# Kernel tuning notes

Measured on AMD Instinct MI355X. Metric: run time of the kernel, lower is better.

Reference implementation:

```python
import jax, jax.numpy as jnp
import numpy as np

H = 64          # hiddens_dims
K = 3           # Chebyshev order
B = 16          # graphs in batch
NPG = 16384     # nodes per graph
N = B * NPG     # total nodes
E = 2_097_152   # total edges
R = 2191        # num_residues (hard-coded in source)
E_REF = R * 16
HALF = N // 2   # backbone count == sidechain count (mask is balanced per graph)


def _lin(k, fan_in, shape):
    return jax.random.uniform(k, shape, jnp.float32, -1.0, 1.0) / np.sqrt(fan_in)


def setup_inputs() -> dict:
    key = jax.random.key(0)
    ks = jax.random.split(key, 40)
    inp = {}
    inp["x"] = jax.random.normal(ks[0], (N, 3), jnp.float32)
    inp["edge_index"] = jax.random.randint(ks[1], (2, E), 0, N)
    inp["batch"] = jnp.repeat(jnp.arange(B, dtype=jnp.int32), NPG)
    blk = jnp.concatenate([jnp.ones((NPG // 2,), bool), jnp.zeros((NPG // 2,), bool)])
    inp["mask"] = jnp.tile(blk, B)  # backbone=True first half of each graph block
    inp["x_ref"] = jax.random.normal(ks[2], (R, 3), jnp.float32)
    inp["edgeref"] = jax.random.randint(ks[3], (2, E_REF), 0, R)
    i = 4
    for name, cin in [("cw0", 3), ("cw1", H), ("cw2", H), ("rw0", 3), ("rw1", H), ("rw2", H)]:
        inp[name] = _lin(ks[i], cin, (K, cin, H)); i += 1
        inp[name.replace("w", "b")] = jnp.zeros((H,), jnp.float32)  # ChebConv bias init = zeros
    for name, cin, cout in [("mlp_w", 2 * H, H), ("mlpP2_w", 2 * H, H),
                            ("rep0_w", H, H), ("rep1_w", H, H), ("rep2_w", H, 3)]:
        inp[name] = _lin(ks[i], cin, (cin, cout)); i += 1
        inp[name.replace("_w", "_b")] = _lin(ks[i], cin, (cout,)); i += 1
    return inp


def cheb_conv(x, edge_index, W, b, n):
    # PyG ChebConv with sym normalization, lambda_max=2: L_hat = -D^-1/2 A D^-1/2 (diag = 0)
    row, col = edge_index[0], edge_index[1]
    deg = jax.ops.segment_sum(jnp.ones_like(x[:, 0])[row] * 0 + 1.0, row, num_segments=n)
    dinv = jnp.where(deg > 0, jax.lax.rsqrt(jnp.maximum(deg, 1e-12)), 0.0)
    w = -(dinv[row] * dinv[col])  # [E]

    def prop(h):  # L_hat @ h via gather + segment_sum
        return jax.ops.segment_sum(w[:, None] * h[col], row, num_segments=n)

    Tx0 = x
    out = Tx0 @ W[0]
    Tx1 = prop(x)
    out = out + Tx1 @ W[1]
    for k in range(2, K):
        Tx2 = 2.0 * prop(Tx1) - Tx0
        out = out + Tx2 @ W[k]
        Tx0, Tx1 = Tx1, Tx2
    return out + b


def _forward(x, edge_index, mask, x_ref, edgeref,
             cw0, cb0, cw1, cb1, cw2, cb2, rw0, rb0, rw1, rb1, rw2, rb2,
             mlp_w, mlp_b, mlpP2_w, mlpP2_b,
             rep0_w, rep0_b, rep1_w, rep1_b, rep2_w, rep2_b):
    # main GNN stack (tanh after all but last; dropout is identity in eval)
    h = jnp.tanh(cheb_conv(x, edge_index, cw0, cb0, N))
    h = jnp.tanh(cheb_conv(h, edge_index, cw1, cb1, N))
    h = cheb_conv(h, edge_index, cw2, cb2, N)

    bb_idx = jnp.nonzero(mask, size=HALF)[0]
    sc_idx = jnp.nonzero(~mask, size=HALF)[0]
    x_bb = h[bb_idx].reshape(B, -1, H).mean(axis=1)[:, None, :]  # [B,1,H]
    x_sc = h[sc_idx].reshape(B, -1, H).mean(axis=1)[:, None, :]  # [B,1,H]

    # reference-graph stack: source bug makes `conv2 != self.convs[-1]` always True,
    # so tanh follows every convRef layer
    r = jnp.tanh(cheb_conv(x_ref, edgeref, rw0, rb0, R))
    r = jnp.tanh(cheb_conv(r, edgeref, rw1, rb1, R))
    r = jnp.tanh(cheb_conv(r, edgeref, rw2, rb2, R))
    r = jnp.broadcast_to(r[None], (B, R, H))

    bb_rep = jnp.broadcast_to(x_bb, (B, R, H))
    phase1 = jnp.concatenate([r, bb_rep], axis=-1) @ mlp_w + mlp_b        # [B,R,H]
    sc_rep = jnp.broadcast_to(x_sc, (B, R, H))
    phase2 = jnp.concatenate([phase1, sc_rep], axis=-1) @ mlpP2_w + mlpP2_b  # [B,R,H]

    res = phase2.reshape(-1, H)
    res = jax.nn.relu(res @ rep0_w + rep0_b)
    res = jax.nn.relu(res @ rep1_w + rep1_b)
    res = jax.nn.relu(res @ rep2_w + rep2_b)  # [B*R, 3]
    return res.reshape(-1, 3), x_bb, x_sc


def reference(x, edge_index, batch, mask, x_ref, edgeref,
              cw0, cb0, cw1, cb1, cw2, cb2, rw0, rb0, rw1, rb1, rw2, rb2,
              mlp_w, mlp_b, mlpP2_w, mlpP2_b,
              rep0_w, rep0_b, rep1_w, rep1_b, rep2_w, rep2_b):
    del batch  # only used for len(batch.unique()) == B, a static constant here
    return _forward(x, edge_index, mask, x_ref, edgeref,
                    cw0, cb0, cw1, cb1, cw2, cb2, rw0, rb0, rw1, rb1, rw2, rb2,
                    mlp_w, mlp_b, mlpP2_w, mlpP2_b,
                    rep0_w, rep0_b, rep1_w, rep1_b, rep2_w, rep2_b)
```

## Files before the change

### kernel.cpp

```cpp
#include <hip/hip_runtime.h>
#include <hip/hip_fp16.h>
#include <math.h>

#define NN 262144
#define NE 2097152
#define RR 2191
#define ER (RR*16)
#define NB 16
#define BRR (NB*RR)
#define OUT_RES (BRR*3)

typedef __attribute__((ext_vector_type(8))) _Float16 half8;
typedef __attribute__((ext_vector_type(4))) float f32x4;

__global__ void k_hist2(const int* __restrict__ eM, int* __restrict__ degM,
                        unsigned char* __restrict__ rankM,
                        const int* __restrict__ eR, int* __restrict__ degR,
                        unsigned char* __restrict__ rankR){
  int b = blockIdx.x;
  if (b < 2048){
    for (int i = b*256 + threadIdx.x; i < NE; i += 2048*256){
      int old = atomicAdd(&degM[eM[i]], 1);
      rankM[i] = (unsigned char)old;
    }
  } else {
    for (int i = (b-2048)*256 + threadIdx.x; i < ER; i += 64*256){
      int old = atomicAdd(&degR[eR[i]], 1);
      rankR[i] = (unsigned char)old;
    }
  }
}

__global__ void k_scan1(const int* __restrict__ deg, int* __restrict__ rowptr,
                        int* __restrict__ partials, float* __restrict__ dinv){
  __shared__ int s[256];
  int t = threadIdx.x; int i = blockIdx.x*256 + t;
  int v = deg[i]; s[t] = v; __syncthreads();
  dinv[i] = v > 0 ? 1.0f/sqrtf((float)v) : 0.0f;
  for (int off = 1; off < 256; off <<= 1){
    int x = (t >= off) ? s[t-off] : 0; __syncthreads();
    s[t] += x; __syncthreads();
  }
  rowptr[i] = s[t] - v;
  if (t == 255) partials[blockIdx.x] = s[255];
}

__global__ void __launch_bounds__(1024) k_scan2m(int* __restrict__ partials,
                                                 const int* __restrict__ degR,
                                                 int* __restrict__ rowptrR,
                                                 float* __restrict__ dinvR){
  __shared__ int s[1024];
  int t = threadIdx.x;
  if (blockIdx.x == 0){
    int v = partials[t]; s[t] = v; __syncthreads();
    for (int off = 1; off < 1024; off <<= 1){
      int x = (t >= off) ? s[t-off] : 0; __syncthreads();
      s[t] += x; __syncthreads();
    }
    partials[t] = s[t] - v;
  } else {
    int carry = 0;
    for (int base = 0; base < RR; base += 1024){
      int idx = base + t;
      int v = (idx < RR) ? degR[idx] : 0;
      if (idx < RR) dinvR[idx] = v > 0 ? 1.0f/sqrtf((float)v) : 0.0f;
      s[t] = v; __syncthreads();
      for (int off = 1; off < 1024; off <<= 1){
        int x = (t >= off) ? s[t-off] : 0; __syncthreads();
        s[t] += x; __syncthreads();
      }
      if (idx < RR) rowptrR[idx] = carry + s[t] - v;
      carry += s[1023];
      __syncthreads();
    }
    if (t == 0) rowptrR[RR] = carry;
  }
}

__global__ void k_scan3(int* __restrict__ rowptr, const int* __restrict__ partials){
  int t = threadIdx.x; int i = blockIdx.x*256 + t;
  rowptr[i] += partials[blockIdx.x];
  if (i == 0) rowptr[NN] = NE;
}

__global__ void k_scatter2(const int* __restrict__ eM, const float* __restrict__ dinv,
                           const int* __restrict__ rowptr, const unsigned char* __restrict__ rankM,
                           int2* __restrict__ pair,
                           const int* __restrict__ eR, const float* __restrict__ dinvR,
                           const int* __restrict__ rowptrR, const unsigned char* __restrict__ rankR,
                           int2* __restrict__ pairR){
  int b = blockIdx.x;
  if (b < 2048){
    for (int i = b*256 + threadIdx.x; i < NE; i += 2048*256){
      int r = eM[i], c = eM[NE + i];
      int pos = rowptr[r] + rankM[i];
      unsigned wbits = (unsigned)__float_as_int(-dinv[r]*dinv[c]);
      long long v = (unsigned)c | ((long long)wbits << 32);
      __builtin_nontemporal_store(v, (long long*)(pair + pos));
    }
  } else {
    for (int i = (b-2048)*256 + threadIdx.x; i < ER; i += 64*256){
      int r = eR[i], c = eR[ER + i];
      int pos = rowptrR[r] + rankR[i];
      unsigned wbits = (unsigned)__float_as_int(-dinvR[r]*dinvR[c]);
      long long v = (unsigned)c | ((long long)wbits << 32);
      __builtin_nontemporal_store(v, (long long*)(pairR + pos));
    }
  }
}

__global__ void k_prep(const float* __restrict__ cw1, const float* __restrict__ cw2,
                       const float* __restrict__ rw1, const float* __restrict__ rw2,
                       float* __restrict__ weffC2, float* __restrict__ weffR1,
                       float* __restrict__ weffR2, _Float16* __restrict__ wfragC1,
                       const float* __restrict__ x, float4* __restrict__ x4,
                       const float* __restrict__ x_ref, float4* __restrict__ xr4){
  int y = blockIdx.y;
  int i = blockIdx.x*blockDim.x + threadIdx.x;
  if (y < 3){
    if (i < 4096){
      const float* W = (y == 0) ? cw2 : (y == 1) ? rw1 : rw2;
      float* D       = (y == 0) ? weffC2 : (y == 1) ? weffR1 : weffR2;
      D[i]        = W[i] - W[8192 + i];
      D[4096 + i] = W[4096 + i];
      D[8192 + i] = 2.0f * W[8192 + i];
    }
  } else if (y == 3){
    if (i < 12288){
      int reg = i & 7, lane = (i >> 3) & 63, nt = (i >> 9) & 3, kc = i >> 11;
      int m = kc >> 1;
      int kin = (kc & 1)*32 + ((lane >> 4) & 3)*8 + reg;
      int n = nt*16 + (lane & 15);
      float eff;
      if      (m == 0) eff = cw1[kin*64 + n] - cw1[8192 + kin*64 + n];
      else if (m == 1) eff = cw1[4096 + kin*64 + n];
      else             eff = 2.0f * cw1[8192 + kin*64 + n];
      wfragC1[i] = (_Float16)eff;
    }
  } else if (y == 4){
    if (i < NN) x4[i] = make_float4(x[i*3], x[i*3+1], x[i*3+2], 0.0f);
  } else {
    if (i < RR) xr4[i] = make_float4(x_ref[i*3], x_ref[i*3+1], x_ref[i*3+2], 0.0f);
  }
}

__global__ void k_prop3p(const float4* __restrict__ h, float4* __restrict__ y,
                         const int* __restrict__ rowptr, const int2* __restrict__ pair, int n){
  int i = blockIdx.x*blockDim.x + threadIdx.x;
  if (i >= n) return;
  float a0 = 0.f, a1 = 0.f, a2 = 0.f;
  int s = rowptr[i], e = rowptr[i+1];
  int p = s;
  for (; p + 4 <= e; p += 4){
    int2 q0 = pair[p], q1 = pair[p+1], q2 = pair[p+2], q3 = pair[p+3];
    float4 v0 = h[q0.x], v1 = h[q1.x], v2 = h[q2.x], v3 = h[q3.x];
    float w0 = __int_as_float(q0.y), w1 = __int_as_float(q1.y);
    float w2 = __int_as_float(q2.y), w3 = __int_as_float(q3.y);
    a0 = fmaf(w0,v0.x, fmaf(w1,v1.x, fmaf(w2,v2.x, fmaf(w3,v3.x, a0))));
    a1 = fmaf(w0,v0.y, fmaf(w1,v1.y, fmaf(w2,v2.y, fmaf(w3,v3.y, a1))));
    a2 = fmaf(w0,v0.z, fmaf(w1,v1.z, fmaf(w2,v2.z, fmaf(w3,v3.z, a2))));
  }
  for (; p < e; p++){
    int2 q = pair[p]; float wv = __int_as_float(q.y);
    float4 v = h[q.x];
    a0 = fmaf(wv, v.x, a0); a1 = fmaf(wv, v.y, a1); a2 = fmaf(wv, v.z, a2);
  }
  y[i] = make_float4(a0, a1, a2, 0.0f);
}

__global__ void k_prop64(const float* __restrict__ h, float* __restrict__ y,
                         const int* __restrict__ rowptr, const int2* __restrict__ pair, int n){
  int t = threadIdx.x, lane = t & 63;
  int i = blockIdx.x*4 + (t >> 6);
  if (i >= n) return;
  float acc = 0.f;
  int s = rowptr[i], e = rowptr[i+1];
  int p = s;
  for (; p + 4 <= e; p += 4){
    int2 q0 = pair[p], q1 = pair[p+1], q2 = pair[p+2], q3 = pair[p+3];
    float v0 = h[(size_t)q0.x*64 + lane], v1 = h[(size_t)q1.x*64 + lane];
    float v2 = h[(size_t)q2.x*64 + lane], v3 = h[(size_t)q3.x*64 + lane];
    acc = fmaf(__int_as_float(q0.y),v0, fmaf(__int_as_float(q1.y),v1,
          fmaf(__int_as_float(q2.y),v2, fmaf(__int_as_float(q3.y),v3, acc))));
  }
  for (; p < e; p++){
    int2 q = pair[p];
    acc = fmaf(__int_as_float(q.y), h[(size_t)q.x*64 + lane], acc);
  }
  y[(size_t)i*64 + lane] = acc;
}

__global__ void __launch_bounds__(256) k_prop64h(
    const uint4* __restrict__ h4, uint4* __restrict__ y4,
    const int* __restrict__ rowptr, const int2* __restrict__ pair, int n){
  int t = threadIdx.x;
  int sub = t & 7;
  int row = blockIdx.x*32 + (t >> 3);
  if (row >= n) return;
  int s = rowptr[row], e = rowptr[row+1];
  float ac[8];
  #pragma unroll
  for (int k = 0; k < 8; k++) ac[k] = 0.f;
  int p = s;
  for (; p + 8 <= e; p += 8){
    int2 q[8]; uint4 v[8];
    #pragma unroll
    for (int j = 0; j < 8; j++) q[j] = pair[p+j];
    #pragma unroll
    for (int j = 0; j < 8; j++) v[j] = h4[(size_t)q[j].x*8 + sub];
    #pragma unroll
    for (int j = 0; j < 8; j++){
      float wv = __int_as_float(q[j].y);
      #pragma unroll
      for (int k = 0; k < 4; k++){
        float2 f = __half22float2(((const __half2*)&v[j])[k]);
        ac[2*k]   = fmaf(wv, f.x, ac[2*k]);
        ac[2*k+1] = fmaf(wv, f.y, ac[2*k+1]);
      }
    }
  }
  for (; p + 4 <= e; p += 4){
    int2 q[4]; uint4 v[4];
    #pragma unroll
    for (int j = 0; j < 4; j++) q[j] = pair[p+j];
    #pragma unroll
    for (int j = 0; j < 4; j++) v[j] = h4[(size_t)q[j].x*8 + sub];
    #pragma unroll
    for (int j = 0; j < 4; j++){
      float wv = __int_as_float(q[j].y);
      #pragma unroll
      for (int k = 0; k < 4; k++){
        float2 f = __half22float2(((const __half2*)&v[j])[k]);
        ac[2*k]   = fmaf(wv, f.x, ac[2*k]);
        ac[2*k+1] = fmaf(wv, f.y, ac[2*k+1]);
      }
    }
  }
  for (; p < e; p++){
    int2 q = pair[p];
    float wv = __int_as_float(q.y);
    uint4 v = h4[(size_t)q.x*8 + sub];
    #pragma unroll
    for (int k = 0; k < 4; k++){
      float2 f = __half22float2(((const __half2*)&v)[k]);
      ac[2*k]   = fmaf(wv, f.x, ac[2*k]);
      ac[2*k+1] = fmaf(wv, f.y, ac[2*k+1]);
    }
  }
  uint4 r;
  #pragma unroll
  for (int k = 0; k < 4; k++){
    __half2 hp = __floats2half2_rn(ac[2*k], ac[2*k+1]);
    ((unsigned*)&r)[k] = *(unsigned*)&hp;
  }
  y4[(size_t)row*8 + sub] = r;
}

__global__ void k_combine3f(const float4* __restrict__ x, const float4* __restrict__ t1,
                            const float4* __restrict__ t2, const float* __restrict__ W,
                            const float* __restrict__ bias, float* __restrict__ out, int n){
  int t = threadIdx.x, lane = t & 63;
  int i = blockIdx.x*4 + (t >> 6);
  if (i >= n) return;
  float4 px = x[i], p1 = t1[i], p2 = t2[i];
  const float* fx = (const float*)&px;
  const float* f1 = (const float*)&p1;
  const float* f2 = (const float*)&p2;
  float acc = bias[lane];
  #pragma unroll
  for (int j = 0; j < 3; j++){
    float x0 = fx[j], x1 = f1[j];
    float x2 = 2.0f*f2[j] - x0;
    acc += x0*W[      j*64 + lane]
         + x1*W[192 + j*64 + lane]
         + x2*W[384 + j*64 + lane];
  }
  out[(size_t)i*64 + lane] = tanhf(acc);
}

__global__ void k_combine3h(const float4* __restrict__ x, const float4* __restrict__ t1,
                            const float4* __restrict__ t2, const float* __restrict__ W,
                            const float* __restrict__ bias, __half* __restrict__ out, int n){
  int t = threadIdx.x, lane = t & 63;
  int i = blockIdx.x*4 + (t >> 6);
  if (i >= n) return;
  float4 px = x[i], p1 = t1[i], p2 = t2[i];
  const float* fx = (const float*)&px;
  const float* f1 = (const float*)&p1;
  const float* f2 = (const float*)&p2;
  float acc = bias[lane];
  #pragma unroll
  for (int j = 0; j < 3; j++){
    float x0 = fx[j], x1 = f1[j];
    float x2 = 2.0f*f2[j] - x0;
    acc += x0*W[      j*64 + lane]
         + x1*W[192 + j*64 + lane]
         + x2*W[384 + j*64 + lane];
  }
  out[(size_t)i*64 + lane] = __float2half_rn(tanhf(acc));
}

__global__ void __launch_bounds__(256) k_combine64m(
    const __half* A, const __half* B, const __half* C,
    const _Float16* __restrict__ wfrag, const float* __restrict__ bias,
    __half* out, int ntiles, int wavestride){
  int t = threadIdx.x;
  int lane = t & 63;
  int wv = blockIdx.x*4 + (t >> 6);
  half8 bf[24];
  #pragma unroll
  for (int i = 0; i < 24; i++)
    bf[i] = *(const half8*)(wfrag + ((size_t)(i*64 + lane))*8);
  int col = lane & 15, grp = (lane >> 4) & 3;
  float b0 = bias[col], b1 = bias[16+col], b2 = bias[32+col], b3 = bias[48+col];
  for (int tile = wv; tile < ntiles; tile += wavestride){
    size_t rb = (size_t)tile*16;
    f32x4 acc0 = {b0,b0,b0,b0}, acc1 = {b1,b1,b1,b1};
    f32x4 acc2 = {b2,b2,b2,b2}, acc3 = {b3,b3,b3,b3};
    #pragma unroll
    for (int kc = 0; kc < 6; kc++){
      const __half* s = (kc < 2) ? A : (kc < 4) ? B : C;
      half8 a = *(const half8*)(s + (rb + col)*64 + (kc & 1)*32 + grp*8);
      acc0 = __builtin_amdgcn_mfma_f32_16x16x32_f16(a, bf[kc*4+0], acc0, 0,0,0);
      acc1 = __builtin_amdgcn_mfma_f32_16x16x32_f16(a, bf[kc*4+1], acc1, 0,0,0);
      acc2 = __builtin_amdgcn_mfma_f32_16x16x32_f16(a, bf[kc*4+2], acc2, 0,0,0);
      acc3 = __builtin_amdgcn_mfma_f32_16x16x32_f16(a, bf[kc*4+3], acc3, 0,0,0);
    }
    __half* o = out + (rb + grp*4)*64;
    #pragma unroll
    for (int r = 0; r < 4; r++){
      o[(size_t)r*64 +      col] = __float2half_rn(tanhf(acc0[r]));
      o[(size_t)r*64 + 16 + col] = __float2half_rn(tanhf(acc1[r]));
      o[(size_t)r*64 + 32 + col] = __float2half_rn(tanhf(acc2[r]));
      o[(size_t)r*64 + 48 + col] = __float2half_rn(tanhf(acc3[r]));
    }
  }
}

__global__ void k_pool3(const __half2* __restrict__ hA, const __half2* __restrict__ hB,
                        const __half2* __restrict__ hC, float* __restrict__ pA,
                        float* __restrict__ pB, float* __restrict__ pC){
  const __half2* src = (blockIdx.y == 0) ? hA : (blockIdx.y == 1) ? hB : hC;
  float* dst         = (blockIdx.y == 0) ? pA : (blockIdx.y == 1) ? pB : pC;
  int blk = blockIdx.x;
  int chunk = blk & 15, seg = blk >> 4;
  int t = threadIdx.x, ch2 = t & 31, rsub = t >> 5;
  int base = seg*8192 + chunk*512;
  float ax = 0.f, ay = 0.f;
  for (int j = 0; j < 64; j++){
    int row = base + rsub + j*8;
    float2 v = __half22float2(src[(size_t)row*32 + ch2]);
    ax += v.x; ay += v.y;
  }
  __shared__ float sx[256], sy[256];
  sx[t] = ax; sy[t] = ay; __syncthreads();
  if (t < 32){
    float tx = 0.f, ty = 0.f;
    #pragma unroll
    for (int j = 0; j < 8; j++){ tx += sx[ch2 + j*32]; ty += sy[ch2 + j*32]; }
    int b = seg >> 1, half_ = seg & 1;
    atomicAdd(&dst[half_*1024 + b*64 + ch2*2],     tx);
    atomicAdd(&dst[half_*1024 + b*64 + ch2*2 + 1], ty);
  }
}

__global__ void k_combine_pooled(const float* __restrict__ pA, const float* __restrict__ pB,
                                 const float* __restrict__ pC, const float* __restrict__ weff,
                                 const float* __restrict__ bias, float* __restrict__ xbbsc,
                                 float* __restrict__ dout){
  int i = blockIdx.x*blockDim.x + threadIdx.x;
  int pr = i >> 6, c = i & 63;
  const float* a = pA + pr*64;
  const float* b = pB + pr*64;
  const float* cc = pC + pr*64;
  float v = 0.f;
  for (int k = 0; k < 64; k++){
    v = fmaf(a[k],  weff[        k*64 + c], v);
    v = fmaf(b[k],  weff[4096 +  k*64 + c], v);
    v = fmaf(cc[k], weff[8192 +  k*64 + c], v);
  }
  v = v*(1.0f/8192.0f) + bias[c];
  xbbsc[i] = v;
  dout[OUT_RES + i] = v;
}

__global__ void __launch_bounds__(256) k_combine64f(
    const float* __restrict__ A, const float* __restrict__ Bm, const float* __restrict__ C,
    const float* __restrict__ Weff, const float* __restrict__ bias,
    float* __restrict__ out, int n){
  int t = threadIdx.x;
  int lane = t & 63;
  int wid  = __builtin_amdgcn_readfirstlane(t >> 6);
  int half_ = wid & 1;
  int row  = blockIdx.x*128 + (wid >> 1)*64 + lane;
  bool active = (row < n);
  float acc[32];
  #pragma unroll
  for (int c = 0; c < 32; c++) acc[c] = bias[half_*32 + c];
  if (active){
    #pragma unroll 1
    for (int m = 0; m < 3; m++){
      const float* src = (m == 0 ? A : (m == 1 ? Bm : C)) + (size_t)row*64;
      const float* Wm  = Weff + m*4096 + half_*32;
      #pragma unroll 1
      for (int k4 = 0; k4 < 16; k4++){
        float4 a4 = *(const float4*)(src + k4*4);
        const float* wk = Wm + k4*256;
        #pragma unroll
        for (int kk = 0; kk < 4; kk++){
          float a = (kk == 0) ? a4.x : (kk == 1) ? a4.y : (kk == 2) ? a4.z : a4.w;
          #pragma unroll
          for (int c = 0; c < 32; c++)
            acc[c] = fmaf(a, wk[kk*64 + c], acc[c]);
        }
      }
    }
  }
  __syncthreads();
  if (active){
    float* o = out + (size_t)row*64 + half_*32;
    #pragma unroll
    for (int c = 0; c < 32; c++) o[c] = tanhf(acc[c]);
  }
}

__global__ void k_refchain(const float* __restrict__ refA, const float* __restrict__ mlp_w,
                           const float* __restrict__ mlp2_w, const float* __restrict__ rep0_w,
                           float* __restrict__ rt3a, int n){
  int t = threadIdx.x, lane = t & 63;
  int i = blockIdx.x*4 + (t >> 6);
  if (i >= n) return;
  float v = refA[i*64 + lane];
  float a = 0.f;
  #pragma unroll
  for (int k = 0; k < 64; k++) a += __shfl(v, k, 64) * mlp_w[k*64 + lane];
  float b = 0.f;
  #pragma unroll
  for (int k = 0; k < 64; k++) b += __shfl(a, k, 64) * mlp2_w[k*64 + lane];
  float c = 0.f;
  #pragma unroll
  for (int k = 0; k < 64; k++) c += __shfl(b, k, 64) * rep0_w[k*64 + lane];
  rt3a[i*64 + lane] = c;
}

__global__ void k_bbchain(const float* __restrict__ xbbsc,
                          const float* __restrict__ mlp_w,  const float* __restrict__ mlp_b,
                          const float* __restrict__ mlp2_w, const float* __restrict__ mlp2_b,
                          const float* __restrict__ rep0_w, const float* __restrict__ rep0_b,
                          float* __restrict__ bt3a){
  int t = threadIdx.x, lane = t & 63;
  int i = blockIdx.x*4 + (t >> 6);
  if (i >= NB) return;
  float vbb = xbbsc[i*64 + lane];
  float vsc = xbbsc[1024 + i*64 + lane];
  float a = mlp_b[lane];
  #pragma unroll
  for (int k = 0; k < 64; k++) a += __shfl(vbb, k, 64) * mlp_w[4096 + k*64 + lane];
  float b = mlp2_b[lane];
  #pragma unroll
  for (int k = 0; k < 64; k++) b += __shfl(a, k, 64) * mlp2_w[k*64 + lane];
  #pragma unroll
  for (int k = 0; k < 64; k++) b += __shfl(vsc, k, 64) * mlp2_w[4096 + k*64 + lane];
  float c = rep0_b[lane];
  #pragma unroll
  for (int k = 0; k < 64; k++) c += __shfl(b, k, 64) * rep0_w[k*64 + lane];
  bt3a[i*64 + lane] = c;
}

__global__ void k_final(const float* __restrict__ rt3, const float* __restrict__ bt3,
                        const float* __restrict__ W1, const float* __restrict__ b1,
                        const float* __restrict__ W2, const float* __restrict__ b2,
                        float* __restrict__ dout){
  int t = threadIdx.x, lane = t & 63;
  int g = blockIdx.x*4 + (t >> 6);
  if (g >= BRR) return;
  int b = g / RR, r = g - b*RR;
  float m = rt3[r*64 + lane] + bt3[b*64 + lane];
  m = fmaxf(m, 0.0f);
  float acc = b1[lane];
  #pragma unroll
  for (int k = 0; k < 64; k++) acc += __shfl(m, k, 64) * W1[k*64 + lane];
  float u = fmaxf(acc, 0.0f);
  float p0 = u*W2[lane*3+0], p1 = u*W2[lane*3+1], p2 = u*W2[lane*3+2];
  #pragma unroll
  for (int off = 32; off > 0; off >>= 1){
    p0 += __shfl_xor(p0, off, 64);
    p1 += __shfl_xor(p1, off, 64);
    p2 += __shfl_xor(p2, off, 64);
  }
  if (lane == 0){
    dout[g*3+0] = fmaxf(p0 + b2[0], 0.0f);
    dout[g*3+1] = fmaxf(p1 + b2[1], 0.0f);
    dout[g*3+2] = fmaxf(p2 + b2[2], 0.0f);
  }
}

extern "C" void kernel_launch(void* const* d_in, const int* in_sizes, int n_in,
                              void* d_out, int out_size, void* d_ws, size_t ws_size,
                              hipStream_t stream){
  const float* x     = (const float*)d_in[0];
  const int*   eidx  = (const int*)d_in[1];
  const float* x_ref = (const float*)d_in[4];
  const int*   eref  = (const int*)d_in[5];
  const float* cw0 = (const float*)d_in[6],  *cb0 = (const float*)d_in[7];
  const float* cw1 = (const float*)d_in[8],  *cb1 = (const float*)d_in[9];
  const float* cw2 = (const float*)d_in[10], *cb2 = (const float*)d_in[11];
  const float* rw0 = (const float*)d_in[12], *rb0 = (const float*)d_in[13];
  const float* rw1 = (const float*)d_in[14], *rb1 = (const float*)d_in[15];
  const float* rw2 = (const float*)d_in[16], *rb2 = (const float*)d_in[17];
  const float* mlp_w  = (const float*)d_in[18], *mlp_b  = (const float*)d_in[19];
  const float* mlp2_w = (const float*)d_in[20], *mlp2_b = (const float*)d_in[21];
  const float* rep0_w = (const float*)d_in[22], *rep0_b = (const float*)d_in[23];
  const float* rep1_w = (const float*)d_in[24], *rep1_b = (const float*)d_in[25];
  const float* rep2_w = (const float*)d_in[26], *rep2_b = (const float*)d_in[27];
  float* out = (float*)d_out;

  char* w = (char*)d_ws;
  size_t off = 0;
  auto alloc = [&](size_t bytes)->void*{
    void* p = w + off;
    off = (off + bytes + 255) & ~(size_t)255;
    return p;
  };
  int*   deg     = (int*)  alloc(NN*4);
  int*   degR    = (int*)  alloc(RR*4);
  float* poolA   = (float*)alloc(2048*4);
  float* poolB   = (float*)alloc(2048*4);
  float* poolC   = (float*)alloc(2048*4);
  size_t zero_bytes = off;

  int*   rowptr   = (int*)  alloc((NN+1)*4);
  int*   partials = (int*)  alloc(1024*4);
  int*   rowptrR  = (int*)  alloc((RR+1)*4);
  float* dinv     = (float*)alloc(NN*4);
  float* dinvR    = (float*)alloc(RR*4);
  unsigned char* rankM = (unsigned char*)alloc(NE);
  unsigned char* rankR = (unsigned char*)alloc(ER);
  int2*  cpair    = (int2*) alloc((size_t)NE*8);
  int2*  cpairR   = (int2*) alloc((size_t)ER*8);
  float4* x4      = (float4*)alloc((size_t)NN*16);
  float4* t1_4    = (float4*)alloc((size_t)NN*16);
  float4* t2_4    = (float4*)alloc((size_t)NN*16);
  float4* xr4     = (float4*)alloc((size_t)RR*16);
  float4* rt1_4   = (float4*)alloc((size_t)RR*16);
  float4* rt2_4   = (float4*)alloc((size_t)RR*16);
  __half* hA      = (__half*)alloc((size_t)NN*64*2);
  __half* hB      = (__half*)alloc((size_t)NN*64*2);
  __half* hC      = (__half*)alloc((size_t)NN*64*2);
  float* refA     = (float*)alloc(RR*64*4);
  float* refB     = (float*)alloc(RR*64*4);
  float* refC     = (float*)alloc(RR*64*4);
  float* xbbsc    = (float*)alloc(2048*4);
  float* rt3a     = (float*)alloc(RR*64*4);
  float* bt3a     = (float*)alloc(NB*64*4);
  float* weffC2   = (float*)alloc(12288*4);
  float* weffR1   = (float*)alloc(12288*4);
  float* weffR2   = (float*)alloc(12288*4);
  _Float16* wfragC1 = (_Float16*)alloc(12288*2);
  (void)ws_size; (void)in_sizes; (void)n_in; (void)out_size;

  hipMemsetAsync(d_ws, 0, zero_bytes, stream);

  k_prep<<<dim3(1024, 6), 256, 0, stream>>>(cw1, cw2, rw1, rw2,
                                            weffC2, weffR1, weffR2, wfragC1,
                                            x, x4, x_ref, xr4);

  k_hist2<<<2112, 256, 0, stream>>>(eidx, deg, rankM, eref, degR, rankR);
  k_scan1<<<1024, 256, 0, stream>>>(deg, rowptr, partials, dinv);
  k_scan2m<<<2, 1024, 0, stream>>>(partials, degR, rowptrR, dinvR);
  k_scan3<<<1024, 256, 0, stream>>>(rowptr, partials);
  k_scatter2<<<2112, 256, 0, stream>>>(eidx, dinv, rowptr, rankM, cpair,
                                       eref, dinvR, rowptrR, rankR, cpairR);

  k_prop3p<<<1024, 256, 0, stream>>>(x4, t1_4, rowptr, cpair, NN);
  k_prop3p<<<1024, 256, 0, stream>>>(t1_4, t2_4, rowptr, cpair, NN);
  k_combine3h<<<NN/4, 256, 0, stream>>>(x4, t1_4, t2_4, cw0, cb0, hA, NN);
  k_prop64h<<<NN/32, 256, 0, stream>>>((const uint4*)hA, (uint4*)hB, rowptr, cpair, NN);
  k_prop64h<<<NN/32, 256, 0, stream>>>((const uint4*)hB, (uint4*)hC, rowptr, cpair, NN);
  k_combine64m<<<1024, 256, 0, stream>>>(hA, hB, hC, wfragC1, cb1, hA, NN/16, 4096);
  k_prop64h<<<NN/32, 256, 0, stream>>>((const uint4*)hA, (uint4*)hB, rowptr, cpair, NN);
  k_prop64h<<<NN/32, 256, 0, stream>>>((const uint4*)hB, (uint4*)hC, rowptr, cpair, NN);
  k_pool3<<<dim3(512,3), 256, 0, stream>>>((const __half2*)hA, (const __half2*)hB,
                                           (const __half2*)hC, poolA, poolB, poolC);
  k_combine_pooled<<<8, 256, 0, stream>>>(poolA, poolB, poolC, weffC2, cb2, xbbsc, out);

  k_prop3p<<<9, 256, 0, stream>>>(xr4, rt1_4, rowptrR, cpairR, RR);
  k_prop3p<<<9, 256, 0, stream>>>(rt1_4, rt2_4, rowptrR, cpairR, RR);
  k_combine3f<<<548, 256, 0, stream>>>(xr4, rt1_4, rt2_4, rw0, rb0, refA, RR);
  k_prop64<<<548, 256, 0, stream>>>(refA, refB, rowptrR, cpairR, RR);
  k_prop64<<<548, 256, 0, stream>>>(refB, refC, rowptrR, cpairR, RR);
  k_combine64f<<<(RR+127)/128, 256, 0, stream>>>(refA, refB, refC, weffR1, rb1, refA, RR);
  k_prop64<<<548, 256, 0, stream>>>(refA, refB, rowptrR, cpairR, RR);
  k_prop64<<<548, 256, 0, stream>>>(refB, refC, rowptrR, cpairR, RR);
  k_combine64f<<<(RR+127)/128, 256, 0, stream>>>(refA, refB, refC, weffR2, rb2, refA, RR);

  k_refchain<<<548, 256, 0, stream>>>(refA, mlp_w, mlp2_w, rep0_w, rt3a, RR);
  k_bbchain<<<4, 256, 0, stream>>>(xbbsc, mlp_w, mlp_b, mlp2_w, mlp2_b, rep0_w, rep0_b, bt3a);

  k_final<<<(BRR+3)/4, 256, 0, stream>>>(rt3a, bt3a, rep1_w, rep1_b, rep2_w, rep2_b, out);
}
```

Before: 724.1 us.

## Merge main-graph and reference-graph kernels into shared launches

Kernels for the large batched graph and the small reference graph that run at the same stage are merged into single launches, with blocks dispatched by block index. The prep work is folded into the histogram kernel in the same way. This cuts the kernel count roughly in half, removing launch overhead and the serialized small reference-graph kernels that left most of the GPU idle. The cost is branchier kernels and possible register-pressure or occupancy changes from combining different bodies.

```diff
diff --git a/kernel.cpp b/kernel.cpp
--- a/kernel.cpp
+++ b/kernel.cpp
@@ -13,21 +13,52 @@
 typedef __attribute__((ext_vector_type(8))) _Float16 half8;
 typedef __attribute__((ext_vector_type(4))) float f32x4;
 
-__global__ void k_hist2(const int* __restrict__ eM, int* __restrict__ degM,
-                        unsigned char* __restrict__ rankM,
-                        const int* __restrict__ eR, int* __restrict__ degR,
-                        unsigned char* __restrict__ rankR){
-  int b = blockIdx.x;
+__global__ void k_histprep(const int* __restrict__ eM, int* __restrict__ degM,
+                           unsigned char* __restrict__ rankM,
+                           const int* __restrict__ eR, int* __restrict__ degR,
+                           unsigned char* __restrict__ rankR,
+                           const float* __restrict__ cw1, const float* __restrict__ cw2,
+                           const float* __restrict__ rw1, const float* __restrict__ rw2,
+                           float* __restrict__ weffC2, float* __restrict__ weffR1,
+                           float* __restrict__ weffR2, _Float16* __restrict__ wfragC1,
+                           const float* __restrict__ x, float4* __restrict__ x4,
+                           const float* __restrict__ x_ref, float4* __restrict__ xr4){
+  int b = blockIdx.x, t = threadIdx.x;
   if (b < 2048){
-    for (int i = b*256 + threadIdx.x; i < NE; i += 2048*256){
+    for (int i = b*256 + t; i < NE; i += 2048*256){
       int old = atomicAdd(&degM[eM[i]], 1);
       rankM[i] = (unsigned char)old;
     }
-  } else {
-    for (int i = (b-2048)*256 + threadIdx.x; i < ER; i += 64*256){
+  } else if (b < 2112){
+    for (int i = (b-2048)*256 + t; i < ER; i += 64*256){
       int old = atomicAdd(&degR[eR[i]], 1);
       rankR[i] = (unsigned char)old;
     }
+  } else if (b < 2160){
+    int y = (b - 2112) >> 4;
+    int i = ((b - 2112) & 15)*256 + t;
+    const float* W = (y == 0) ? cw2 : (y == 1) ? rw1 : rw2;
+    float* D       = (y == 0) ? weffC2 : (y == 1) ? weffR1 : weffR2;
+    D[i]        = W[i] - W[8192 + i];
+    D[4096 + i] = W[4096 + i];
+    D[8192 + i] = 2.0f * W[8192 + i];
+  } else if (b < 2208){
+    int i = (b - 2160)*256 + t;
+    int reg = i & 7, lane = (i >> 3) & 63, nt = (i >> 9) & 3, kc = i >> 11;
+    int m = kc >> 1;
+    int kin = (kc & 1)*32 + ((lane >> 4) & 3)*8 + reg;
+    int n = nt*16 + (lane & 15);
+    float eff;
+    if      (m == 0) eff = cw1[kin*64 + n] - cw1[8192 + kin*64 + n];
+    else if (m == 1) eff = cw1[4096 + kin*64 + n];
+    else             eff = 2.0f * cw1[8192 + kin*64 + n];
+    wfragC1[i] = (_Float16)eff;
+  } else if (b < 3232){
+    int i = (b - 2208)*256 + t;
+    if (i < NN) x4[i] = make_float4(x[i*3], x[i*3+1], x[i*3+2], 0.0f);
+  } else {
+    int i = (b - 3232)*256 + t;
+    if (i < RR) xr4[i] = make_float4(x_ref[i*3], x_ref[i*3+1], x_ref[i*3+2], 0.0f);
   }
 }
 
@@ -109,45 +140,9 @@
   }
 }
 
-__global__ void k_prep(const float* __restrict__ cw1, const float* __restrict__ cw2,
-                       const float* __restrict__ rw1, const float* __restrict__ rw2,
-                       float* __restrict__ weffC2, float* __restrict__ weffR1,
-                       float* __restrict__ weffR2, _Float16* __restrict__ wfragC1,
-                       const float* __restrict__ x, float4* __restrict__ x4,
-                       const float* __restrict__ x_ref, float4* __restrict__ xr4){
-  int y = blockIdx.y;
-  int i = blockIdx.x*blockDim.x + threadIdx.x;
-  if (y < 3){
-    if (i < 4096){
-      const float* W = (y == 0) ? cw2 : (y == 1) ? rw1 : rw2;
-      float* D       = (y == 0) ? weffC2 : (y == 1) ? weffR1 : weffR2;
-      D[i]        = W[i] - W[8192 + i];
-      D[4096 + i] = W[4096 + i];
-      D[8192 + i] = 2.0f * W[8192 + i];
-    }
-  } else if (y == 3){
-    if (i < 12288){
-      int reg = i & 7, lane = (i >> 3) & 63, nt = (i >> 9) & 3, kc = i >> 11;
-      int m = kc >> 1;
-      int kin = (kc & 1)*32 + ((lane >> 4) & 3)*8 + reg;
-      int n = nt*16 + (lane & 15);
-      float eff;
-      if      (m == 0) eff = cw1[kin*64 + n] - cw1[8192 + kin*64 + n];
-      else if (m == 1) eff = cw1[4096 + kin*64 + n];
-      else             eff = 2.0f * cw1[8192 + kin*64 + n];
-      wfragC1[i] = (_Float16)eff;
-    }
-  } else if (y == 4){
-    if (i < NN) x4[i] = make_float4(x[i*3], x[i*3+1], x[i*3+2], 0.0f);
-  } else {
-    if (i < RR) xr4[i] = make_float4(x_ref[i*3], x_ref[i*3+1], x_ref[i*3+2], 0.0f);
-  }
-}
-
-__global__ void k_prop3p(const float4* __restrict__ h, float4* __restrict__ y,
-                         const int* __restrict__ rowptr, const int2* __restrict__ pair, int n){
-  int i = blockIdx.x*blockDim.x + threadIdx.x;
-  if (i >= n) return;
+__device__ __forceinline__ void prop3_body(const float4* __restrict__ h, float4* __restrict__ y,
+                                           const int* __restrict__ rowptr,
+                                           const int2* __restrict__ pair, int i){
   float a0 = 0.f, a1 = 0.f, a2 = 0.f;
   int s = rowptr[i], e = rowptr[i+1];
   int p = s;
@@ -168,11 +163,31 @@
   y[i] = make_float4(a0, a1, a2, 0.0f);
 }
 
-__global__ void k_prop64(const float* __restrict__ h, float* __restrict__ y,
-                         const int* __restrict__ rowptr, const int2* __restrict__ pair, int n){
-  int t = threadIdx.x, lane = t & 63;
-  int i = blockIdx.x*4 + (t >> 6);
-  if (i >= n) return;
+__device__ __forceinline__ void combine3_body(const float4* __restrict__ x,
+                                              const float4* __restrict__ t1,
+                                              const float4* __restrict__ t2,
+                                              const float* __restrict__ W,
+                                              const float* __restrict__ bias,
+                                              int i, int lane, float* accout){
+  float4 px = x[i], p1 = t1[i], p2 = t2[i];
+  const float* fx = (const float*)&px;
+  const float* f1 = (const float*)&p1;
+  const float* f2 = (const float*)&p2;
+  float acc = bias[lane];
+  #pragma unroll
+  for (int j = 0; j < 3; j++){
+    float x0 = fx[j], x1 = f1[j];
+    float x2 = 2.0f*f2[j] - x0;
+    acc += x0*W[      j*64 + lane]
+         + x1*W[192 + j*64 + lane]
+         + x2*W[384 + j*64 + lane];
+  }
+  *accout = tanhf(acc);
+}
+
+__device__ __forceinline__ void prop64f_body(const float* __restrict__ h, float* __restrict__ y,
+                                             const int* __restrict__ rowptr,
+                                             const int2* __restrict__ pair, int i, int lane){
   float acc = 0.f;
   int s = rowptr[i], e = rowptr[i+1];
   int p = s;
@@ -190,209 +205,17 @@
   y[(size_t)i*64 + lane] = acc;
 }
 
-__global__ void __launch_bounds__(256) k_prop64h(
-    const uint4* __restrict__ h4, uint4* __restrict__ y4,
-    const int* __restrict__ rowptr, const int2* __restrict__ pair, int n){
-  int t = threadIdx.x;
-  int sub = t & 7;
-  int row = blockIdx.x*32 + (t >> 3);
-  if (row >= n) return;
-  int s = rowptr[row], e = rowptr[row+1];
-  float ac[8];
-  #pragma unroll
-  for (int k = 0; k < 8; k++) ac[k] = 0.f;
-  int p = s;
-  for (; p + 8 <= e; p += 8){
-    int2 q[8]; uint4 v[8];
-    #pragma unroll
-    for (int j = 0; j < 8; j++) q[j] = pair[p+j];
-    #pragma unroll
-    for (int j = 0; j < 8; j++) v[j] = h4[(size_t)q[j].x*8 + sub];
-    #pragma unroll
-    for (int j = 0; j < 8; j++){
-      float wv = __int_as_float(q[j].y);
-      #pragma unroll
-      for (int k = 0; k < 4; k++){
-        float2 f = __half22float2(((const __half2*)&v[j])[k]);
-        ac[2*k]   = fmaf(wv, f.x, ac[2*k]);
-        ac[2*k+1] = fmaf(wv, f.y, ac[2*k+1]);
-      }
-    }
-  }
-  for (; p + 4 <= e; p += 4){
-    int2 q[4]; uint4 v[4];
-    #pragma unroll
-    for (int j = 0; j < 4; j++) q[j] = pair[p+j];
-    #pragma unroll
-    for (int j = 0; j < 4; j++) v[j] = h4[(size_t)q[j].x*8 + sub];
-    #pragma unroll
-    for (int j = 0; j < 4; j++){
-      float wv = __int_as_float(q[j].y);
-      #pragma unroll
-      for (int k = 0; k < 4; k++){
-        float2 f = __half22float2(((const __half2*)&v[j])[k]);
-        ac[2*k]   = fmaf(wv, f.x, ac[2*k]);
-        ac[2*k+1] = fmaf(wv, f.y, ac[2*k+1]);
-      }
-    }
-  }
-  for (; p < e; p++){
-    int2 q = pair[p];
-    float wv = __int_as_float(q.y);
-    uint4 v = h4[(size_t)q.x*8 + sub];
-    #pragma unroll
-    for (int k = 0; k < 4; k++){
-      float2 f = __half22float2(((const __half2*)&v)[k]);
-      ac[2*k]   = fmaf(wv, f.x, ac[2*k]);
-      ac[2*k+1] = fmaf(wv, f.y, ac[2*k+1]);
-    }
-  }
-  uint4 r;
-  #pragma unroll
-  for (int k = 0; k < 4; k++){
-    __half2 hp = __floats2half2_rn(ac[2*k], ac[2*k+1]);
-    ((unsigned*)&r)[k] = *(unsigned*)&hp;
-  }
-  y4[(size_t)row*8 + sub] = r;
-}
-
-__global__ void k_combine3f(const float4* __restrict__ x, const float4* __restrict__ t1,
-                            const float4* __restrict__ t2, const float* __restrict__ W,
-                            const float* __restrict__ bias, float* __restrict__ out, int n){
-  int t = threadIdx.x, lane = t & 63;
-  int i = blockIdx.x*4 + (t >> 6);
-  if (i >= n) return;
-  float4 px = x[i], p1 = t1[i], p2 = t2[i];
-  const float* fx = (const float*)&px;
-  const float* f1 = (const float*)&p1;
-  const float* f2 = (const float*)&p2;
-  float acc = bias[lane];
-  #pragma unroll
-  for (int j = 0; j < 3; j++){
-    float x0 = fx[j], x1 = f1[j];
-    float x2 = 2.0f*f2[j] - x0;
-    acc += x0*W[      j*64 + lane]
-         + x1*W[192 + j*64 + lane]
-         + x2*W[384 + j*64 + lane];
-  }
-  out[(size_t)i*64 + lane] = tanhf(acc);
-}
-
-__global__ void k_combine3h(const float4* __restrict__ x, const float4* __restrict__ t1,
-                            const float4* __restrict__ t2, const float* __restrict__ W,
-                            const float* __restrict__ bias, __half* __restrict__ out, int n){
-  int t = threadIdx.x, lane = t & 63;
-  int i = blockIdx.x*4 + (t >> 6);
-  if (i >= n) return;
-  float4 px = x[i], p1 = t1[i], p2 = t2[i];
-  const float* fx = (const float*)&px;
-  const float* f1 = (const float*)&p1;
-  const float* f2 = (const float*)&p2;
-  float acc = bias[lane];
-  #pragma unroll
-  for (int j = 0; j < 3; j++){
-    float x0 = fx[j], x1 = f1[j];
-    float x2 = 2.0f*f2[j] - x0;
-    acc += x0*W[      j*64 + lane]
-         + x1*W[192 + j*64 + lane]
-         + x2*W[384 + j*64 + lane];
-  }
-  out[(size_t)i*64 + lane] = __float2half_rn(tanhf(acc));
-}
-
-__global__ void __launch_bounds__(256) k_combine64m(
-    const __half* A, const __half* B, const __half* C,
-    const _Float16* __restrict__ wfrag, const float* __restrict__ bias,
-    __half* out, int ntiles, int wavestride){
-  int t = threadIdx.x;
-  int lane = t & 63;
-  int wv = blockIdx.x*4 + (t >> 6);
-  half8 bf[24];
-  #pragma unroll
-  for (int i = 0; i < 24; i++)
-    bf[i] = *(const half8*)(wfrag + ((size_t)(i*64 + lane))*8);
-  int col = lane & 15, grp = (lane >> 4) & 3;
-  float b0 = bias[col], b1 = bias[16+col], b2 = bias[32+col], b3 = bias[48+col];
-  for (int tile = wv; tile < ntiles; tile += wavestride){
-    size_t rb = (size_t)tile*16;
-    f32x4 acc0 = {b0,b0,b0,b0}, acc1 = {b1,b1,b1,b1};
-    f32x4 acc2 = {b2,b2,b2,b2}, acc3 = {b3,b3,b3,b3};
-    #pragma unroll
-    for (int kc = 0; kc < 6; kc++){
-      const __half* s = (kc < 2) ? A : (kc < 4) ? B : C;
-      half8 a = *(const half8*)(s + (rb + col)*64 + (kc & 1)*32 + grp*8);
-      acc0 = __builtin_amdgcn_mfma_f32_16x16x32_f16(a, bf[kc*4+0], acc0, 0,0,0);
-      acc1 = __builtin_amdgcn_mfma_f32_16x16x32_f16(a, bf[kc*4+1], acc1, 0,0,0);
-      acc2 = __builtin_amdgcn_mfma_f32_16x16x32_f16(a, bf[kc*4+2], acc2, 0,0,0);
-      acc3 = __builtin_amdgcn_mfma_f32_16x16x32_f16(a, bf[kc*4+3], acc3, 0,0,0);
-    }
-    __half* o = out + (rb + grp*4)*64;
-    #pragma unroll
-    for (int r = 0; r < 4; r++){
-      o[(size_t)r*64 +      col] = __float2half_rn(tanhf(acc0[r]));
-      o[(size_t)r*64 + 16 + col] = __float2half_rn(tanhf(acc1[r]));
-      o[(size_t)r*64 + 32 + col] = __float2half_rn(tanhf(acc2[r]));
-      o[(size_t)r*64 + 48 + col] = __float2half_rn(tanhf(acc3[r]));
-    }
-  }
-}
-
-__global__ void k_pool3(const __half2* __restrict__ hA, const __half2* __restrict__ hB,
-                        const __half2* __restrict__ hC, float* __restrict__ pA,
-                        float* __restrict__ pB, float* __restrict__ pC){
-  const __half2* src = (blockIdx.y == 0) ? hA : (blockIdx.y == 1) ? hB : hC;
-  float* dst         = (blockIdx.y == 0) ? pA : (blockIdx.y == 1) ? pB : pC;
-  int blk = blockIdx.x;
-  int chunk = blk & 15, seg = blk >> 4;
-  int t = threadIdx.x, ch2 = t & 31, rsub = t >> 5;
-  int base = seg*8192 + chunk*512;
-  float ax = 0.f, ay = 0.f;
-  for (int j = 0; j < 64; j++){
-    int row = base + rsub + j*8;
-    float2 v = __half22float2(src[(size_t)row*32 + ch2]);
-    ax += v.x; ay += v.y;
-  }
-  __shared__ float sx[256], sy[256];
-  sx[t] = ax; sy[t] = ay; __syncthreads();
-  if (t < 32){
-    float tx = 0.f, ty = 0.f;
-    #pragma unroll
-    for (int j = 0; j < 8; j++){ tx += sx[ch2 + j*32]; ty += sy[ch2 + j*32]; }
-    int b = seg >> 1, half_ = seg & 1;
-    atomicAdd(&dst[half_*1024 + b*64 + ch2*2],     tx);
-    atomicAdd(&dst[half_*1024 + b*64 + ch2*2 + 1], ty);
-  }
-}
-
-__global__ void k_combine_pooled(const float* __restrict__ pA, const float* __restrict__ pB,
-                                 const float* __restrict__ pC, const float* __restrict__ weff,
-                                 const float* __restrict__ bias, float* __restrict__ xbbsc,
-                                 float* __restrict__ dout){
-  int i = blockIdx.x*blockDim.x + threadIdx.x;
-  int pr = i >> 6, c = i & 63;
-  const float* a = pA + pr*64;
-  const float* b = pB + pr*64;
-  const float* cc = pC + pr*64;
-  float v = 0.f;
-  for (int k = 0; k < 64; k++){
-    v = fmaf(a[k],  weff[        k*64 + c], v);
-    v = fmaf(b[k],  weff[4096 +  k*64 + c], v);
-    v = fmaf(cc[k], weff[8192 +  k*64 + c], v);
-  }
-  v = v*(1.0f/8192.0f) + bias[c];
-  xbbsc[i] = v;
-  dout[OUT_RES + i] = v;
-}
-
-__global__ void __launch_bounds__(256) k_combine64f(
-    const float* __restrict__ A, const float* __restrict__ Bm, const float* __restrict__ C,
-    const float* __restrict__ Weff, const float* __restrict__ bias,
-    float* __restrict__ out, int n){
-  int t = threadIdx.x;
+__device__ __forceinline__ void combine64f_body(const float* __restrict__ A,
+                                                const float* __restrict__ Bm,
+                                                const float* __restrict__ C,
+                                                const float* __restrict__ Weff,
+                                                const float* __restrict__ bias,
+                                                float* __restrict__ out, int n,
+                                                int blk, int t){
   int lane = t & 63;
   int wid  = __builtin_amdgcn_readfirstlane(t >> 6);
   int half_ = wid & 1;
-  int row  = blockIdx.x*128 + (wid >> 1)*64 + lane;
+  int row  = blk*128 + (wid >> 1)*64 + lane;
   bool active = (row < n);
   float acc[32];
   #pragma unroll
@@ -424,23 +247,230 @@
   }
 }
 
-__global__ void k_refchain(const float* __restrict__ refA, const float* __restrict__ mlp_w,
-                           const float* __restrict__ mlp2_w, const float* __restrict__ rep0_w,
-                           float* __restrict__ rt3a, int n){
-  int t = threadIdx.x, lane = t & 63;
-  int i = blockIdx.x*4 + (t >> 6);
-  if (i >= n) return;
-  float v = refA[i*64 + lane];
-  float a = 0.f;
-  #pragma unroll
-  for (int k = 0; k < 64; k++) a += __shfl(v, k, 64) * mlp_w[k*64 + lane];
-  float b = 0.f;
-  #pragma unroll
-  for (int k = 0; k < 64; k++) b += __shfl(a, k, 64) * mlp2_w[k*64 + lane];
-  float c = 0.f;
-  #pragma unroll
-  for (int k = 0; k < 64; k++) c += __shfl(b, k, 64) * rep0_w[k*64 + lane];
-  rt3a[i*64 + lane] = c;
+__global__ void k_prop3m(const float4* __restrict__ hM, float4* __restrict__ yM,
+                         const int* __restrict__ rowptr, const int2* __restrict__ pair,
+                         const float4* __restrict__ hR, float4* __restrict__ yR,
+                         const int* __restrict__ rowptrR, const int2* __restrict__ pairR){
+  int b = blockIdx.x, t = threadIdx.x;
+  if (b < 1024){
+    prop3_body(hM, yM, rowptr, pair, b*256 + t);
+  } else {
+    int i = (b - 1024)*256 + t;
+    if (i < RR) prop3_body(hR, yR, rowptrR, pairR, i);
+  }
+}
+
+__global__ void k_combine3m(const float4* __restrict__ x, const float4* __restrict__ t1,
+                            const float4* __restrict__ t2, const float* __restrict__ cW,
+                            const float* __restrict__ cb, __half* __restrict__ outM,
+                            const float4* __restrict__ xr, const float4* __restrict__ r1,
+                            const float4* __restrict__ r2, const float* __restrict__ rW,
+                            const float* __restrict__ rb, float* __restrict__ outR){
+  int b = blockIdx.x, t = threadIdx.x, lane = t & 63;
+  if (b < 65536){
+    int i = b*4 + (t >> 6);
+    float v; combine3_body(x, t1, t2, cW, cb, i, lane, &v);
+    outM[(size_t)i*64 + lane] = __float2half_rn(v);
+  } else {
+    int i = (b - 65536)*4 + (t >> 6);
+    if (i < RR){
+      float v; combine3_body(xr, r1, r2, rW, rb, i, lane, &v);
+      outR[(size_t)i*64 + lane] = v;
+    }
+  }
+}
+
+__global__ void __launch_bounds__(256) k_prop64m(
+    const uint4* __restrict__ h4, uint4* __restrict__ y4,
+    const int* __restrict__ rowptr, const int2* __restrict__ pair,
+    const float* __restrict__ hR, float* __restrict__ yR,
+    const int* __restrict__ rowptrR, const int2* __restrict__ pairR){
+  int b = blockIdx.x, t = threadIdx.x;
+  if (b >= 8192){
+    int i = (b - 8192)*4 + (t >> 6);
+    if (i < RR) prop64f_body(hR, yR, rowptrR, pairR, i, t & 63);
+    return;
+  }
+  int sub = t & 7;
+  int row = b*32 + (t >> 3);
+  int s = rowptr[row], e = rowptr[row+1];
+  float ac[8];
+  #pragma unroll
+  for (int k = 0; k < 8; k++) ac[k] = 0.f;
+  int p = s;
+  for (; p + 8 <= e; p += 8){
+    int2 q[8]; uint4 v[8];
+    #pragma unroll
+    for (int j = 0; j < 8; j++) q[j] = pair[p+j];
+    #pragma unroll
+    for (int j = 0; j < 8; j++) v[j] = h4[(size_t)q[j].x*8 + sub];
+    #pragma unroll
+    for (int j = 0; j < 8; j++){
+      float wv = __int_as_float(q[j].y);
+      #pragma unroll
+      for (int k = 0; k < 4; k++){
+        float2 f = __half22float2(((const __half2*)&v[j])[k]);
+        ac[2*k]   = fmaf(wv, f.x, ac[2*k]);
+        ac[2*k+1] = fmaf(wv, f.y, ac[2*k+1]);
+      }
+    }
+  }
+  for (; p + 4 <= e; p += 4){
+    int2 q[4]; uint4 v[4];
+    #pragma unroll
+    for (int j = 0; j < 4; j++) q[j] = pair[p+j];
+    #pragma unroll
+    for (int j = 0; j < 4; j++) v[j] = h4[(size_t)q[j].x*8 + sub];
+    #pragma unroll
+    for (int j = 0; j < 4; j++){
+      float wv = __int_as_float(q[j].y);
+      #pragma unroll
+      for (int k = 0; k < 4; k++){
+        float2 f = __half22float2(((const __half2*)&v[j])[k]);
+        ac[2*k]   = fmaf(wv, f.x, ac[2*k]);
+        ac[2*k+1] = fmaf(wv, f.y, ac[2*k+1]);
+      }
+    }
+  }
+  for (; p < e; p++){
+    int2 q = pair[p];
+    float wv = __int_as_float(q.y);
+    uint4 v = h4[(size_t)q.x*8 + sub];
+    #pragma unroll
+    for (int k = 0; k < 4; k++){
+      float2 f = __half22float2(((const __half2*)&v)[k]);
+      ac[2*k]   = fmaf(wv, f.x, ac[2*k]);
+      ac[2*k+1] = fmaf(wv, f.y, ac[2*k+1]);
+    }
+  }
+  uint4 r;
+  #pragma unroll
+  for (int k = 0; k < 4; k++){
+    __half2 hp = __floats2half2_rn(ac[2*k], ac[2*k+1]);
+    ((unsigned*)&r)[k] = *(unsigned*)&hp;
+  }
+  y4[(size_t)row*8 + sub] = r;
+}
+
+__global__ void __launch_bounds__(256) k_combine64mm(
+    const __half* A, const __half* B, const __half* C,
+    const _Float16* __restrict__ wfrag, const float* __restrict__ bias,
+    __half* out, int ntiles, int wavestride,
+    const float* __restrict__ rA, const float* __restrict__ rB, const float* __restrict__ rC,
+    const float* __restrict__ weffR, const float* __restrict__ biasR,
+    float* __restrict__ outR){
+  int t = threadIdx.x;
+  if (blockIdx.x >= 1024){
+    combine64f_body(rA, rB, rC, weffR, biasR, outR, RR, blockIdx.x - 1024, t);
+    return;
+  }
+  int lane = t & 63;
+  int wv = blockIdx.x*4 + (t >> 6);
+  half8 bf[24];
+  #pragma unroll
+  for (int i = 0; i < 24; i++)
+    bf[i] = *(const half8*)(wfrag + ((size_t)(i*64 + lane))*8);
+  int col = lane & 15, grp = (lane >> 4) & 3;
+  float b0 = bias[col], b1 = bias[16+col], b2 = bias[32+col], b3 = bias[48+col];
+  for (int tile = wv; tile < ntiles; tile += wavestride){
+    size_t rb = (size_t)tile*16;
+    f32x4 acc0 = {b0,b0,b0,b0}, acc1 = {b1,b1,b1,b1};
+    f32x4 acc2 = {b2,b2,b2,b2}, acc3 = {b3,b3,b3,b3};
+    #pragma unroll
+    for (int kc = 0; kc < 6; kc++){
+      const __half* s = (kc < 2) ? A : (kc < 4) ? B : C;
+      half8 a = *(const half8*)(s + (rb + col)*64 + (kc & 1)*32 + grp*8);
+      acc0 = __builtin_amdgcn_mfma_f32_16x16x32_f16(a, bf[kc*4+0], acc0, 0,0,0);
+      acc1 = __builtin_amdgcn_mfma_f32_16x16x32_f16(a, bf[kc*4+1], acc1, 0,0,0);
+      acc2 = __builtin_amdgcn_mfma_f32_16x16x32_f16(a, bf[kc*4+2], acc2, 0,0,0);
+      acc3 = __builtin_amdgcn_mfma_f32_16x16x32_f16(a, bf[kc*4+3], acc3, 0,0,0);
+    }
+    __half* o = out + (rb + grp*4)*64;
+    #pragma unroll
+    for (int r = 0; r < 4; r++){
+      o[(size_t)r*64 +      col] = __float2half_rn(tanhf(acc0[r]));
+      o[(size_t)r*64 + 16 + col] = __float2half_rn(tanhf(acc1[r]));
+      o[(size_t)r*64 + 32 + col] = __float2half_rn(tanhf(acc2[r]));
+      o[(size_t)r*64 + 48 + col] = __float2half_rn(tanhf(acc3[r]));
+    }
+  }
+}
+
+__global__ void k_tail3(const __half2* __restrict__ hA, const __half2* __restrict__ hB,
+                        const __half2* __restrict__ hC, float* __restrict__ pA,
+                        float* __restrict__ pB, float* __restrict__ pC,
+                        const float* __restrict__ rA, const float* __restrict__ rB,
+                        const float* __restrict__ rC, const float* __restrict__ weffR,
+                        const float* __restrict__ biasR, float* __restrict__ outR){
+  int b = blockIdx.x, t = threadIdx.x;
+  if (b >= 1536){
+    combine64f_body(rA, rB, rC, weffR, biasR, outR, RR, b - 1536, t);
+    return;
+  }
+  int y = b >> 9;
+  const __half2* src = (y == 0) ? hA : (y == 1) ? hB : hC;
+  float* dst         = (y == 0) ? pA : (y == 1) ? pB : pC;
+  int blk = b & 511;
+  int chunk = blk & 15, seg = blk >> 4;
+  int ch2 = t & 31, rsub = t >> 5;
+  int base = seg*8192 + chunk*512;
+  float ax = 0.f, ay = 0.f;
+  for (int j = 0; j < 64; j++){
+    int row = base + rsub + j*8;
+    float2 v = __half22float2(src[(size_t)row*32 + ch2]);
+    ax += v.x; ay += v.y;
+  }
+  __shared__ float sx[256], sy[256];
+  sx[t] = ax; sy[t] = ay; __syncthreads();
+  if (t < 32){
+    float tx = 0.f, ty = 0.f;
+    #pragma unroll
+    for (int j = 0; j < 8; j++){ tx += sx[ch2 + j*32]; ty += sy[ch2 + j*32]; }
+    int bb = seg >> 1, half_ = seg & 1;
+    atomicAdd(&dst[half_*1024 + bb*64 + ch2*2],     tx);
+    atomicAdd(&dst[half_*1024 + bb*64 + ch2*2 + 1], ty);
+  }
+}
+
+__global__ void k_cpr(const float* __restrict__ pA, const float* __restrict__ pB,
+                      const float* __restrict__ pC, const float* __restrict__ weff,
+                      const float* __restrict__ bias, float* __restrict__ xbbsc,
+                      float* __restrict__ dout,
+                      const float* __restrict__ refA, const float* __restrict__ mlp_w,
+                      const float* __restrict__ mlp2_w, const float* __restrict__ rep0_w,
+                      float* __restrict__ rt3a){
+  int b = blockIdx.x, t = threadIdx.x;
+  if (b < 8){
+    int i = b*256 + t;
+    int pr = i >> 6, c = i & 63;
+    const float* a = pA + pr*64;
+    const float* bb = pB + pr*64;
+    const float* cc = pC + pr*64;
+    float v = 0.f;
+    for (int k = 0; k < 64; k++){
+      v = fmaf(a[k],  weff[        k*64 + c], v);
+      v = fmaf(bb[k], weff[4096 +  k*64 + c], v);
+      v = fmaf(cc[k], weff[8192 +  k*64 + c], v);
+    }
+    v = v*(1.0f/8192.0f) + bias[c];
+    xbbsc[i] = v;
+    dout[OUT_RES + i] = v;
+  } else {
+    int lane = t & 63;
+    int i = (b - 8)*4 + (t >> 6);
+    if (i >= RR) return;
+    float v = refA[i*64 + lane];
+    float a = 0.f;
+    #pragma unroll
+    for (int k = 0; k < 64; k++) a += __shfl(v, k, 64) * mlp_w[k*64 + lane];
+    float bb = 0.f;
+    #pragma unroll
+    for (int k = 0; k < 64; k++) bb += __shfl(a, k, 64) * mlp2_w[k*64 + lane];
+    float c = 0.f;
+    #pragma unroll
+    for (int k = 0; k < 64; k++) c += __shfl(bb, k, 64) * rep0_w[k*64 + lane];
+    rt3a[i*64 + lane] = c;
+  }
 }
 
 __global__ void k_bbchain(const float* __restrict__ xbbsc,
@@ -561,41 +591,35 @@
 
   hipMemsetAsync(d_ws, 0, zero_bytes, stream);
 
-  k_prep<<<dim3(1024, 6), 256, 0, stream>>>(cw1, cw2, rw1, rw2,
-                                            weffC2, weffR1, weffR2, wfragC1,
-                                            x, x4, x_ref, xr4);
-
-  k_hist2<<<2112, 256, 0, stream>>>(eidx, deg, rankM, eref, degR, rankR);
+  k_histprep<<<3241, 256, 0, stream>>>(eidx, deg, rankM, eref, degR, rankR,
+                                       cw1, cw2, rw1, rw2,
+                                       weffC2, weffR1, weffR2, wfragC1,
+                                       x, x4, x_ref, xr4);
   k_scan1<<<1024, 256, 0, stream>>>(deg, rowptr, partials, dinv);
   k_scan2m<<<2, 1024, 0, stream>>>(partials, degR, rowptrR, dinvR);
   k_scan3<<<1024, 256, 0, stream>>>(rowptr, partials);
   k_scatter2<<<2112, 256, 0, stream>>>(eidx, dinv, rowptr, rankM, cpair,
                                        eref, dinvR, rowptrR, rankR, cpairR);
 
-  k_prop3p<<<1024, 256, 0, stream>>>(x4, t1_4, rowptr, cpair, NN);
-  k_prop3p<<<1024, 256, 0, stream>>>(t1_4, t2_4, rowptr, cpair, NN);
-  k_combine3h<<<NN/4, 256, 0, stream>>>(x4, t1_4, t2_4, cw0, cb0, hA, NN);
-  k_prop64h<<<NN/32, 256, 0, stream>>>((const uint4*)hA, (uint4*)hB, rowptr, cpair, NN);
-  k_prop64h<<<NN/32, 256, 0, stream>>>((const uint4*)hB, (uint4*)hC, rowptr, cpair, NN);
-  k_combine64m<<<1024, 256, 0, stream>>>(hA, hB, hC, wfragC1, cb1, hA, NN/16, 4096);
-  k_prop64h<<<NN/32, 256, 0, stream>>>((const uint4*)hA, (uint4*)hB, rowptr, cpair, NN);
-  k_prop64h<<<NN/32, 256, 0, stream>>>((const uint4*)hB, (uint4*)hC, rowptr, cpair, NN);
-  k_pool3<<<dim3(512,3), 256, 0, stream>>>((const __half2*)hA, (const __half2*)hB,
-                                           (const __half2*)hC, poolA, poolB, poolC);
-  k_combine_pooled<<<8, 256, 0, stream>>>(poolA, poolB, poolC, weffC2, cb2, xbbsc, out);
-
-  k_prop3p<<<9, 256, 0, stream>>>(xr4, rt1_4, rowptrR, cpairR, RR);
-  k_prop3p<<<9, 256, 0, stream>>>(rt1_4, rt2_4, rowptrR, cpairR, RR);
-  k_combine3f<<<548, 256, 0, stream>>>(xr4, rt1_4, rt2_4, rw0, rb0, refA, RR);
-  k_prop64<<<548, 256, 0, stream>>>(refA, refB, rowptrR, cpairR, RR);
-  k_prop64<<<548, 256, 0, stream>>>(refB, refC, rowptrR, cpairR, RR);
-  k_combine64f<<<(RR+127)/128, 256, 0, stream>>>(refA, refB, refC, weffR1, rb1, refA, RR);
-  k_prop64<<<548, 256, 0, stream>>>(refA, refB, rowptrR, cpairR, RR);
-  k_prop64<<<548, 256, 0, stream>>>(refB, refC, rowptrR, cpairR, RR);
-  k_combine64f<<<(RR+127)/128, 256, 0, stream>>>(refA, refB, refC, weffR2, rb2, refA, RR);
-
-  k_refchain<<<548, 256, 0, stream>>>(refA, mlp_w, mlp2_w, rep0_w, rt3a, RR);
+  k_prop3m<<<1033, 256, 0, stream>>>(x4, t1_4, rowptr, cpair, xr4, rt1_4, rowptrR, cpairR);
+  k_prop3m<<<1033, 256, 0, stream>>>(t1_4, t2_4, rowptr, cpair, rt1_4, rt2_4, rowptrR, cpairR);
+  k_combine3m<<<66084, 256, 0, stream>>>(x4, t1_4, t2_4, cw0, cb0, hA,
+                                         xr4, rt1_4, rt2_4, rw0, rb0, refA);
+  k_prop64m<<<8740, 256, 0, stream>>>((const uint4*)hA, (uint4*)hB, rowptr, cpair,
+                                      refA, refB, rowptrR, cpairR);
+  k_prop64m<<<8740, 256, 0, stream>>>((const uint4*)hB, (uint4*)hC, rowptr, cpair,
+                                      refB, refC, rowptrR, cpairR);
+  k_combine64mm<<<1042, 256, 0, stream>>>(hA, hB, hC, wfragC1, cb1, hA, NN/16, 4096,
+                                          refA, refB, refC, weffR1, rb1, refA);
+  k_prop64m<<<8740, 256, 0, stream>>>((const uint4*)hA, (uint4*)hB, rowptr, cpair,
+                                      refA, refB, rowptrR, cpairR);
+  k_prop64m<<<8740, 256, 0, stream>>>((const uint4*)hB, (uint4*)hC, rowptr, cpair,
+                                      refB, refC, rowptrR, cpairR);
+  k_tail3<<<1554, 256, 0, stream>>>((const __half2*)hA, (const __half2*)hB, (const __half2*)hC,
+                                    poolA, poolB, poolC,
+                                    refA, refB, refC, weffR2, rb2, refA);
+  k_cpr<<<556, 256, 0, stream>>>(poolA, poolB, poolC, weffC2, cb2, xbbsc, out,
+                                 refA, mlp_w, mlp2_w, rep0_w, rt3a);
   k_bbchain<<<4, 256, 0, stream>>>(xbbsc, mlp_w, mlp_b, mlp2_w, mlp2_b, rep0_w, rep0_b, bt3a);
-
   k_final<<<(BRR+3)/4, 256, 0, stream>>>(rt3a, bt3a, rep1_w, rep1_b, rep2_w, rep2_b, out);
 }
```

Result: faster. 673.1 us (-7.0%).
